# Kernel optimization log

Measured on AMD Instinct MI355X. Metric: run time of the kernel, lower is better.

The kernel has to match this reference:

```python
import jax, jax.numpy as jnp
import numpy as np

N, E, A = 10000, 160000, 8
P, ATTR = 30000, 64
EMB, HID, HEADS = 128, 128, 4
OUT, NF, NR = 64, 1500, 64
HOPS = 3
NEG = -1e30


def _gatv2(x, src, dst, e_emb, node_mask, Wl, Wr, We, att, b):
    """GATv2Conv with edge features, self-loops (edge attr = mean of kept edges),
    restricted to the node subset given by node_mask (mirrors Data.subgraph)."""
    n = x.shape[0]
    H, D = att.shape
    xl = (x @ Wl).reshape(n, H, D)
    xr = (x @ Wr).reshape(n, H, D)
    emask = node_mask[src] & node_mask[dst]
    w = emask.astype(x.dtype)
    mean_e = (e_emb * w[:, None]).sum(0) / jnp.maximum(w.sum(), 1.0)  # fill_value='mean'
    loops = jnp.arange(n)
    src_a = jnp.concatenate([src, loops])
    dst_a = jnp.concatenate([dst, loops])
    e_a = jnp.concatenate([e_emb, jnp.broadcast_to(mean_e, (n, e_emb.shape[1]))], axis=0)
    m_a = jnp.concatenate([emask, node_mask])
    ee = (e_a @ We).reshape(-1, H, D)
    z = jax.nn.leaky_relu(xl[src_a] + xr[dst_a] + ee, 0.2)  # [E+N, H, D]
    s = jnp.einsum('ehd,hd->eh', z, att)
    s = jnp.where(m_a[:, None], s, NEG)
    smax = jax.ops.segment_max(s, dst_a, num_segments=n)
    ex = jnp.exp(s - smax[dst_a]) * m_a[:, None].astype(x.dtype)
    den = jax.ops.segment_sum(ex, dst_a, num_segments=n)
    alpha = ex / (den[dst_a] + 1e-16)
    out = jax.ops.segment_sum(alpha[:, :, None] * xl[src_a], dst_a, num_segments=n)
    return out.reshape(n, H * D) + b


def _softmax_aggr(x, mask):
    # PyG SoftmaxAggregation (t=1): per-channel softmax over nodes, weighted sum.
    logit = jnp.where(mask[:, None], x, NEG)
    return jnp.einsum('nd,nd->d', jax.nn.softmax(logit, axis=0), x)


def _khop(seed, src, dst):
    # k_hop_subgraph, flow='source_to_target': grow node set backwards along edges.
    m = jnp.zeros(N, dtype=bool).at[seed].set(True)
    for _ in range(HOPS):
        reach = jnp.zeros(N, dtype=jnp.int32).at[src].max(m[dst].astype(jnp.int32))
        m = m | (reach > 0)
    return m


def _forward(node_pred, edge_index, edge_attr, arg_nodes, pred_emb, Wl1, Wr1, We1, att1, b1,
             Wl2, Wr2, We2, att2, b2, kqv_f, kqvb_f, kqv_r, kqvb_r, a_rel, m_rel, p_rel,
             aW_f, ab_f, aW_r, ab_r, Wfr, bfr, Wro, bro):
    src, dst = edge_index[0], edge_index[1]
    p_emb = pred_emb[node_pred]   # [N, EMB]
    a_emb = pred_emb[edge_attr]   # [E, EMB] (original uses predicate_embedding for attrs)
    full = jnp.ones(N, dtype=bool)
    h = _gatv2(p_emb, src, dst, a_emb, full, Wl1, Wr1, We1, att1, b1)  # [N, HID*HEADS]
    frame_x = _softmax_aggr(h, full)                                   # [512]
    masks = jax.vmap(lambda s: _khop(s, src, dst))(arg_nodes)          # [A, N]
    role_list = []
    for i in range(A):  # mirrors the original Python loop over root args (A fixed, small)
        hi = _gatv2(h, src, dst, a_emb, masks[i], Wl2, Wr2, We2, att2, b2)
        role_list.append(_softmax_aggr(hi, masks[i]))
    role_x = jnp.stack(role_list)                                      # [A, 512]
    # HGTConv, heads=1. Edge types: 0=f-loop, 1=frame->role, 2=r-loop.
    sq = 1.0 / np.sqrt(OUT)
    kf = frame_x @ kqv_f[0] + kqvb_f[0]
    vf = frame_x @ kqv_f[2] + kqvb_f[2]
    kr = role_x @ kqv_r[0] + kqvb_r[0]
    qr = role_x @ kqv_r[1] + kqvb_r[1]
    vr = role_x @ kqv_r[2] + kqvb_r[2]
    # frame dst has a single incoming edge (f-loop) -> softmax weight is exactly 1
    agg_f = vf @ m_rel[0]
    # role dst: softmax over {frame->role edge, role self-loop}
    s_fr = (qr * (kf @ a_rel[1])[None, :]).sum(-1) * sq * p_rel[1]  # [A]
    s_rr = (qr * (kr @ a_rel[2])).sum(-1) * sq * p_rel[2]           # [A]
    al = jax.nn.softmax(jnp.stack([s_fr, s_rr], axis=1), axis=1)    # [A, 2]
    agg_r = al[:, 0:1] * (vf @ m_rel[1])[None, :] + al[:, 1:2] * (vr @ m_rel[2])
    # in_dim (512) != out_dim (64) -> no residual skip in PyG HGTConv
    out_f = jax.nn.gelu(agg_f, approximate=False) @ aW_f + ab_f
    out_r = jax.nn.gelu(agg_r, approximate=False) @ aW_r + ab_r
    frame = jax.nn.log_softmax(out_f @ Wfr + bfr)
    roles = jax.nn.log_softmax(out_r @ Wro + bro, axis=-1)
    return frame, roles


def setup_inputs() -> dict:
    key = jax.random.key(0)
    ki = iter(jax.random.split(key, 32))
    def nrm(shape, fan):
        return (jax.random.normal(next(ki), shape, jnp.float32) / np.sqrt(fan)).astype(jnp.float32)
    D1 = HID * HEADS
    inp = {
        'node_pred': jax.random.randint(next(ki), (N,), 0, P),
        'edge_index': jax.random.randint(next(ki), (2, E), 0, N),
        'edge_attr': jax.random.randint(next(ki), (E,), 0, ATTR),
        'arg_nodes': jax.random.randint(next(ki), (A,), 0, N),
        'pred_emb': nrm((P, EMB), 1.0),
        'Wl1': nrm((EMB, D1), EMB), 'Wr1': nrm((EMB, D1), EMB), 'We1': nrm((EMB, D1), EMB),
        'att1': nrm((HEADS, HID), HID), 'b1': jnp.zeros((D1,), jnp.float32),
        'Wl2': nrm((D1, D1), D1), 'Wr2': nrm((D1, D1), D1), 'We2': nrm((EMB, D1), EMB),
        'att2': nrm((HEADS, HID), HID), 'b2': jnp.zeros((D1,), jnp.float32),
        'kqv_f': nrm((3, D1, OUT), D1), 'kqvb_f': jnp.zeros((3, OUT), jnp.float32),
        'kqv_r': nrm((3, D1, OUT), D1), 'kqvb_r': jnp.zeros((3, OUT), jnp.float32),
        'a_rel': nrm((3, OUT, OUT), OUT), 'm_rel': nrm((3, OUT, OUT), OUT),
        'p_rel': jnp.ones((3,), jnp.float32),
        'aW_f': nrm((OUT, OUT), OUT), 'ab_f': jnp.zeros((OUT,), jnp.float32),
        'aW_r': nrm((OUT, OUT), OUT), 'ab_r': jnp.zeros((OUT,), jnp.float32),
        'Wfr': nrm((OUT, NF), OUT), 'bfr': jnp.zeros((NF,), jnp.float32),
        'Wro': nrm((OUT, NR), OUT), 'bro': jnp.zeros((NR,), jnp.float32),
    }
    return inp


def reference(node_pred, edge_index, edge_attr, arg_nodes, pred_emb, Wl1, Wr1, We1, att1, b1,
              Wl2, Wr2, We2, att2, b2, kqv_f, kqvb_f, kqv_r, kqvb_r, a_rel, m_rel, p_rel,
              aW_f, ab_f, aW_r, ab_r, Wfr, bfr, Wro, bro):
    return _forward(node_pred, edge_index, edge_attr, arg_nodes, pred_emb, Wl1, Wr1, We1, att1, b1,
                    Wl2, Wr2, We2, att2, b2, kqv_f, kqvb_f, kqv_r, kqvb_r, a_rel, m_rel, p_rel,
                    aW_f, ab_f, aW_r, ab_r, Wfr, bfr, Wro, bro)
```

## Files before the change

### kernel.cpp

```cpp
#include <hip/hip_runtime.h>
#include <cfloat>
#include <cmath>

static constexpr int NN   = 10000;
static constexpr int NE   = 160000;
static constexpr int NA   = 8;
static constexpr int D1   = 512;
static constexpr int EMBD = 128;
static constexpr int NATTR= 64;
static constexpr int OUTD = 64;
static constexpr int NFR  = 1500;
static constexpr int AGG_NB = 250;

typedef short bf16x8 __attribute__((ext_vector_type(8)));
typedef float f32x4  __attribute__((ext_vector_type(4)));

__device__ __forceinline__ float b2f(unsigned short u) {
    union { unsigned u; float f; } v; v.u = ((unsigned)u) << 16; return v.f;
}
__device__ __forceinline__ unsigned short f2b(float f) {
    union { float f; unsigned u; } v; v.f = f;
    unsigned r = v.u + 0x7FFFu + ((v.u >> 16) & 1u);
    return (unsigned short)(r >> 16);
}

__global__ void k_cast_all(const float* __restrict__ W1, const float* __restrict__ W2,
                           const float* __restrict__ W3, const float* __restrict__ W4,
                           unsigned short* __restrict__ o1, unsigned short* __restrict__ o2,
                           unsigned short* __restrict__ o3, unsigned short* __restrict__ o4) {
    int i = blockIdx.x * blockDim.x + threadIdx.x;
    const int n1 = EMBD * D1 / 4;
    const int n2 = D1 * D1 / 4;
    const float* src; unsigned short* dst; int off;
    if (i < n1)                { src = W1; dst = o1; off = i; }
    else if (i < 2 * n1)       { src = W2; dst = o2; off = i - n1; }
    else if (i < 2 * n1 + n2)  { src = W3; dst = o3; off = i - 2 * n1; }
    else if (i < 2 * n1 + 2 * n2) { src = W4; dst = o4; off = i - 2 * n1 - n2; }
    else return;
    float4 v = ((const float4*)src)[off];
    ushort4 o; o.x = f2b(v.x); o.y = f2b(v.y); o.z = f2b(v.z); o.w = f2b(v.w);
    ((ushort4*)dst)[off] = o;
}

__global__ void k_gather_pemb(const int* __restrict__ node_pred,
                              const float* __restrict__ pred_emb,
                              unsigned short* __restrict__ pemb) {
    int idx = blockIdx.x * blockDim.x + threadIdx.x;
    int total = NN * (EMBD / 4);
    if (idx >= total) return;
    int n = idx >> 5, j = idx & 31;
    float4 v = ((const float4*)(pred_emb + (size_t)node_pred[n] * EMBD))[j];
    ushort4 o; o.x = f2b(v.x); o.y = f2b(v.y); o.z = f2b(v.z); o.w = f2b(v.w);
    ((ushort4*)(pemb + (size_t)n * EMBD))[j] = o;
}

__global__ void k_attr_ee(const float* __restrict__ pred_emb,
                          const float* __restrict__ We1, const float* __restrict__ We2,
                          unsigned short* __restrict__ t1, unsigned short* __restrict__ t2) {
    int a = blockIdx.x & 63;
    int which = blockIdx.x >> 6;
    const float* We = which ? We2 : We1;
    unsigned short* out = which ? t2 : t1;
    __shared__ float row[EMBD];
    if (threadIdx.x < EMBD) row[threadIdx.x] = pred_emb[a * EMBD + threadIdx.x];
    __syncthreads();
    int c = threadIdx.x;
    float acc = 0.f;
    for (int k = 0; k < EMBD; ++k) acc += row[k] * We[k * D1 + c];
    out[a * D1 + c] = f2b(acc);
}

__global__ void k_indeg(const int* __restrict__ dst, int* __restrict__ counts) {
    int stride = gridDim.x * blockDim.x;
    for (int e = blockIdx.x * blockDim.x + threadIdx.x; e < NE; e += stride)
        atomicAdd(&counts[dst[e]], 1);
}

__global__ __launch_bounds__(1024) void k_scan(const int* __restrict__ counts,
                                               int* __restrict__ row_ptr,
                                               int* __restrict__ cursor) {
    __shared__ int s[1024];
    __shared__ int base_s;
    int t = threadIdx.x;
    if (t == 0) base_s = 0;
    __syncthreads();
    for (int c0 = 0; c0 < NN; c0 += 1024) {
        int v = (c0 + t < NN) ? counts[c0 + t] : 0;
        s[t] = v; __syncthreads();
        for (int off = 1; off < 1024; off <<= 1) {
            int add = (t >= off) ? s[t - off] : 0;
            __syncthreads();
            s[t] += add;
            __syncthreads();
        }
        int base = base_s;
        int excl = base + s[t] - v;
        if (c0 + t < NN) { row_ptr[c0 + t] = excl; cursor[c0 + t] = excl; }
        __syncthreads();
        if (t == 0) base_s = base + s[1023];
        __syncthreads();
    }
    if (t == 0) row_ptr[NN] = base_s;
}

__global__ void k_scatter(const int* __restrict__ src, const int* __restrict__ dst,
                          const int* __restrict__ attr, int* __restrict__ cursor,
                          int* __restrict__ csr_src, int* __restrict__ csr_attr) {
    int stride = gridDim.x * blockDim.x;
    for (int e = blockIdx.x * blockDim.x + threadIdx.x; e < NE; e += stride) {
        int pos = atomicAdd(&cursor[dst[e]], 1);
        csr_src[pos] = src[e];
        csr_attr[pos] = attr[e];
    }
}

__global__ void k_mask_seed(const int* __restrict__ arg_nodes, unsigned* __restrict__ mask) {
    if (threadIdx.x < NA) atomicOr(&mask[arg_nodes[threadIdx.x]], 1u << threadIdx.x);
}

__global__ void k_prop(const unsigned* __restrict__ oldm, unsigned* __restrict__ newm,
                       const int* __restrict__ src, const int* __restrict__ dst) {
    int stride = gridDim.x * blockDim.x;
    int t0 = blockIdx.x * blockDim.x + threadIdx.x;
    for (int n = t0; n < NN; n += stride) atomicOr(&newm[n], oldm[n]);
    for (int e = t0; e < NE; e += stride) {
        unsigned v = oldm[dst[e]];
        if (v) atomicOr(&newm[src[e]], v);
    }
}

__global__ void k_hist(const int* __restrict__ src, const int* __restrict__ dst,
                       const int* __restrict__ attr, const unsigned* __restrict__ mask,
                       unsigned* __restrict__ hist) {
    __shared__ unsigned lh[9 * 64];
    for (int i = threadIdx.x; i < 9 * 64; i += blockDim.x) lh[i] = 0;
    __syncthreads();
    int stride = gridDim.x * blockDim.x;
    for (int e = blockIdx.x * blockDim.x + threadIdx.x; e < NE; e += stride) {
        int a = attr[e] & 63;
        atomicAdd(&lh[a], 1u);
        unsigned bits = mask[src[e]] & mask[dst[e]];
        while (bits) {
            int i = __ffs(bits) - 1;
            bits &= bits - 1;
            atomicAdd(&lh[(1 + i) * 64 + a], 1u);
        }
    }
    __syncthreads();
    for (int i = threadIdx.x; i < 9 * 64; i += blockDim.x)
        if (lh[i]) atomicAdd(&hist[i], lh[i]);
}

__global__ __launch_bounds__(512) void k_mean_ee(const unsigned* __restrict__ hist,
                                                 const float* __restrict__ pred_emb,
                                                 const float* __restrict__ We1,
                                                 const float* __restrict__ We2,
                                                 unsigned short* __restrict__ mee1,
                                                 unsigned short* __restrict__ mee2) {
    int g = blockIdx.x;
    const float* We = (g == 0) ? We1 : We2;
    unsigned short* out = (g == 0) ? mee1 : (mee2 + (g - 1) * D1);
    __shared__ float cnt[64];
    __shared__ float me[EMBD];
    __shared__ float tot_s;
    if (threadIdx.x < 64) cnt[threadIdx.x] = (float)hist[g * 64 + threadIdx.x];
    __syncthreads();
    if (threadIdx.x == 0) {
        float tt = 0.f;
        for (int a = 0; a < 64; ++a) tt += cnt[a];
        tot_s = fmaxf(tt, 1.0f);
    }
    __syncthreads();
    if (threadIdx.x < EMBD) {
        float acc = 0.f;
        for (int a = 0; a < 64; ++a) acc += cnt[a] * pred_emb[a * EMBD + threadIdx.x];
        me[threadIdx.x] = acc / tot_s;
    }
    __syncthreads();
    int c = threadIdx.x;
    float acc = 0.f;
    for (int k = 0; k < EMBD; ++k) acc += me[k] * We[k * D1 + c];
    out[c] = f2b(acc);
}

__global__ __launch_bounds__(256) void k_gemm_dual(const unsigned short* __restrict__ A,
                                                   const unsigned short* __restrict__ B0,
                                                   const unsigned short* __restrict__ B1,
                                                   unsigned short* __restrict__ C0,
                                                   unsigned short* __restrict__ C1,
                                                   int M, int K, int N) {
    const unsigned short* B = blockIdx.z ? B1 : B0;
    unsigned short* C = blockIdx.z ? C1 : C0;
    __shared__ unsigned short As[64][40];
    __shared__ unsigned short Bs[64][40];
    int tid = threadIdx.x;
    int wave = tid >> 6, lane = tid & 63;
    int bm = blockIdx.y * 64, bn = blockIdx.x * 64;
    int wr = (wave >> 1) * 32, wc = (wave & 1) * 32;
    f32x4 zero = {0.f, 0.f, 0.f, 0.f};
    f32x4 acc[2][2] = {{zero, zero}, {zero, zero}};
    for (int k0 = 0; k0 < K; k0 += 32) {
#pragma unroll
        for (int i = 0; i < 4; ++i) {
            int idx = tid + 256 * i;
            int row = idx >> 4, kp = (idx & 15) * 2;
            unsigned v = 0;
            if (bm + row < M) v = *(const unsigned*)&A[(size_t)(bm + row) * K + k0 + kp];
            *(unsigned*)&As[row][kp] = v;
        }
#pragma unroll
        for (int i = 0; i < 8; ++i) {
            int idx = tid + 256 * i;
            int k = idx >> 6, n = idx & 63;
            Bs[n][k] = B[(size_t)(k0 + k) * N + bn + n];
        }
        __syncthreads();
        int r = lane & 15, kb = (lane >> 4) * 8;
        bf16x8 a0 = *(const bf16x8*)&As[wr + r][kb];
        bf16x8 a1 = *(const bf16x8*)&As[wr + 16 + r][kb];
        bf16x8 b0 = *(const bf16x8*)&Bs[wc + r][kb];
        bf16x8 b1 = *(const bf16x8*)&Bs[wc + 16 + r][kb];
        acc[0][0] = __builtin_amdgcn_mfma_f32_16x16x32_bf16(a0, b0, acc[0][0], 0, 0, 0);
        acc[0][1] = __builtin_amdgcn_mfma_f32_16x16x32_bf16(a0, b1, acc[0][1], 0, 0, 0);
        acc[1][0] = __builtin_amdgcn_mfma_f32_16x16x32_bf16(a1, b0, acc[1][0], 0, 0, 0);
        acc[1][1] = __builtin_amdgcn_mfma_f32_16x16x32_bf16(a1, b1, acc[1][1], 0, 0, 0);
        __syncthreads();
    }
    int cr = (lane >> 4) * 4, cc = lane & 15;
#pragma unroll
    for (int i = 0; i < 2; ++i)
#pragma unroll
        for (int j = 0; j < 2; ++j)
#pragma unroll
            for (int q = 0; q < 4; ++q) {
                int row = bm + wr + i * 16 + cr + q;
                int col = bn + wc + j * 16 + cc;
                if (row < M) C[(size_t)row * N + col] = f2b(acc[i][j][q]);
            }
}

__global__ __launch_bounds__(256) void k_gat(const unsigned short* __restrict__ xl,
                                             const unsigned short* __restrict__ xr,
                                             const unsigned short* __restrict__ attr_ee,
                                             const unsigned short* __restrict__ mean_ee,
                                             const float* __restrict__ att,
                                             const float* __restrict__ bias,
                                             const int* __restrict__ row_ptr,
                                             const int* __restrict__ csr_src,
                                             const int* __restrict__ csr_attr,
                                             unsigned short* __restrict__ out) {
    int n = blockIdx.x;
    int t = threadIdx.x;
    int c = 2 * t;
    unsigned vr_ = *(const unsigned*)&xr[(size_t)n * D1 + c];
    float xr0 = b2f((unsigned short)(vr_ & 0xffff));
    float xr1 = b2f((unsigned short)(vr_ >> 16));
    float a0 = att[c], a1 = att[c + 1];
    float m = -FLT_MAX, den = 0.f, acc0 = 0.f, acc1 = 0.f;
    int pstart = row_ptr[n], pend = row_ptr[n + 1];
    int deg = pend - pstart;
    int items = deg + 1;
    for (int it = 0; it < items; it += 4) {
        float xs0[4], xs1[4], ps[4];
#pragma unroll
        for (int u = 0; u < 4; ++u) {
            int item = it + u;
            bool valid = item < items;
            int s; const unsigned short* ee;
            if (!valid || item == deg) { s = n; ee = mean_ee; }
            else {
                int p = pstart + item;
                s = csr_src[p];
                ee = attr_ee + (size_t)(csr_attr[p] & 63) * D1;
            }
            unsigned vs = *(const unsigned*)&xl[(size_t)s * D1 + c];
            unsigned ve = *(const unsigned*)&ee[c];
            float x0 = b2f((unsigned short)(vs & 0xffff));
            float x1 = b2f((unsigned short)(vs >> 16));
            float z0 = x0 + xr0 + b2f((unsigned short)(ve & 0xffff));
            float z1 = x1 + xr1 + b2f((unsigned short)(ve >> 16));
            z0 = (z0 > 0.f) ? z0 : 0.2f * z0;
            z1 = (z1 > 0.f) ? z1 : 0.2f * z1;
            xs0[u] = x0; xs1[u] = x1;
            ps[u] = z0 * a0 + z1 * a1;
        }
#pragma unroll
        for (int off = 32; off; off >>= 1) {
#pragma unroll
            for (int u = 0; u < 4; ++u) ps[u] += __shfl_xor(ps[u], off, 64);
        }
#pragma unroll
        for (int u = 0; u < 4; ++u) if (it + u >= items) ps[u] = -FLT_MAX;
        float nm = fmaxf(fmaxf(fmaxf(ps[0], ps[1]), fmaxf(ps[2], ps[3])), m);
        float sc = __expf(m - nm);
        float w0 = __expf(ps[0] - nm);
        float w1 = __expf(ps[1] - nm);
        float w2 = __expf(ps[2] - nm);
        float w3 = __expf(ps[3] - nm);
        den  = den * sc + ((w0 + w1) + (w2 + w3));
        acc0 = acc0 * sc + ((w0 * xs0[0] + w1 * xs0[1]) + (w2 * xs0[2] + w3 * xs0[3]));
        acc1 = acc1 * sc + ((w0 * xs1[0] + w1 * xs1[1]) + (w2 * xs1[2] + w3 * xs1[3]));
        m = nm;
    }
    float inv = 1.f / (den + 1e-16f);
    unsigned short o0 = f2b(acc0 * inv + bias[c]);
    unsigned short o1 = f2b(acc1 * inv + bias[c + 1]);
    *(unsigned*)&out[(size_t)n * D1 + c] = ((unsigned)o1 << 16) | o0;
}

__global__ __launch_bounds__(256) void k_gat_m4(const unsigned short* __restrict__ xl,
                                                const unsigned short* __restrict__ xr,
                                                const unsigned short* __restrict__ attr_ee,
                                                const unsigned short* __restrict__ mee,
                                                const float* __restrict__ att,
                                                const float* __restrict__ bias,
                                                const int* __restrict__ row_ptr,
                                                const int* __restrict__ csr_src,
                                                const int* __restrict__ csr_attr,
                                                const unsigned* __restrict__ mask, int bitbase,
                                                unsigned short* __restrict__ o0,
                                                unsigned short* __restrict__ o1,
                                                unsigned short* __restrict__ o2,
                                                unsigned short* __restrict__ o3) {
    int n = blockIdx.x;
    unsigned mb_n = (mask[n] >> bitbase) & 0xFu;
    if (!mb_n) return;
    __shared__ int lst[256];
    __shared__ int lcnt;
    int t = threadIdx.x, lane = t & 63;
    int c = 2 * t;
    unsigned vr_ = *(const unsigned*)&xr[(size_t)n * D1 + c];
    float xr0 = b2f((unsigned short)(vr_ & 0xffff));
    float xr1 = b2f((unsigned short)(vr_ >> 16));
    float a0 = att[c], a1 = att[c + 1];
    float m[4], den[4], ac0[4], ac1[4];
#pragma unroll
    for (int b = 0; b < 4; ++b) { m[b] = -FLT_MAX; den[b] = 0.f; ac0[b] = 0.f; ac1[b] = 0.f; }
    int pstart = row_ptr[n], pend = row_ptr[n + 1];
    for (int p0 = pstart; p0 < pend; p0 += 256) {
        int chunk = min(256, pend - p0);
        __syncthreads();
        if (t == 0) lcnt = 0;
        __syncthreads();
        unsigned bits = 0; int sv = 0, av = 0;
        if (t < chunk) {
            int p = p0 + t;
            sv = csr_src[p];
            av = csr_attr[p] & 63;
            bits = (mask[sv] >> bitbase) & mb_n & 0xFu;
        }
        bool kept = bits != 0;
        unsigned long long bal = __ballot(kept);
        int base = 0;
        if (lane == 0) base = atomicAdd(&lcnt, __popcll(bal));
        base = __shfl(base, 0, 64);
        int pfx = __popcll(bal & ((1ull << lane) - 1));
        if (kept) lst[base + pfx] = sv | (av << 14) | ((int)bits << 20);
        __syncthreads();
        int cnt = lcnt;
        int i = 0;
        for (; i + 1 < cnt; i += 2) {
            int vA = lst[i], vB = lst[i + 1];
            int sA = vA & 0x3FFF, sB = vB & 0x3FFF;
            unsigned bA = ((unsigned)vA >> 20) & 0xF, bB = ((unsigned)vB >> 20) & 0xF;
            const unsigned short* eA = attr_ee + (size_t)((vA >> 14) & 63) * D1;
            const unsigned short* eB = attr_ee + (size_t)((vB >> 14) & 63) * D1;
            unsigned vsA = *(const unsigned*)&xl[(size_t)sA * D1 + c];
            unsigned veA = *(const unsigned*)&eA[c];
            unsigned vsB = *(const unsigned*)&xl[(size_t)sB * D1 + c];
            unsigned veB = *(const unsigned*)&eB[c];
            float xA0 = b2f((unsigned short)(vsA & 0xffff)), xA1 = b2f((unsigned short)(vsA >> 16));
            float xB0 = b2f((unsigned short)(vsB & 0xffff)), xB1 = b2f((unsigned short)(vsB >> 16));
            float zA0 = xA0 + xr0 + b2f((unsigned short)(veA & 0xffff));
            float zA1 = xA1 + xr1 + b2f((unsigned short)(veA >> 16));
            float zB0 = xB0 + xr0 + b2f((unsigned short)(veB & 0xffff));
            float zB1 = xB1 + xr1 + b2f((unsigned short)(veB >> 16));
            zA0 = (zA0 > 0.f) ? zA0 : 0.2f * zA0;
            zA1 = (zA1 > 0.f) ? zA1 : 0.2f * zA1;
            zB0 = (zB0 > 0.f) ? zB0 : 0.2f * zB0;
            zB1 = (zB1 > 0.f) ? zB1 : 0.2f * zB1;
            float pa = zA0 * a0 + zA1 * a1;
            float pb = zB0 * a0 + zB1 * a1;
#pragma unroll
            for (int off = 32; off; off >>= 1) {
                pa += __shfl_xor(pa, off, 64);
                pb += __shfl_xor(pb, off, 64);
            }
#pragma unroll
            for (int b = 0; b < 4; ++b) {
                if (!(((bA | bB) >> b) & 1)) continue;
                float pae = ((bA >> b) & 1) ? pa : -FLT_MAX;
                float pbe = ((bB >> b) & 1) ? pb : -FLT_MAX;
                float nm = fmaxf(m[b], fmaxf(pae, pbe));
                float sc = __expf(m[b] - nm);
                float wa = __expf(pae - nm);
                float wb = __expf(pbe - nm);
                den[b] = den[b] * sc + wa + wb;
                ac0[b] = ac0[b] * sc + wa * xA0 + wb * xB0;
                ac1[b] = ac1[b] * sc + wa * xA1 + wb * xB1;
                m[b] = nm;
            }
        }
        if (i < cnt) {
            int vA = lst[i];
            int sA = vA & 0x3FFF;
            unsigned bA = ((unsigned)vA >> 20) & 0xF;
            const unsigned short* eA = attr_ee + (size_t)((vA >> 14) & 63) * D1;
            unsigned vsA = *(const unsigned*)&xl[(size_t)sA * D1 + c];
            unsigned veA = *(const unsigned*)&eA[c];
            float xA0 = b2f((unsigned short)(vsA & 0xffff)), xA1 = b2f((unsigned short)(vsA >> 16));
            float zA0 = xA0 + xr0 + b2f((unsigned short)(veA & 0xffff));
            float zA1 = xA1 + xr1 + b2f((unsigned short)(veA >> 16));
            zA0 = (zA0 > 0.f) ? zA0 : 0.2f * zA0;
            zA1 = (zA1 > 0.f) ? zA1 : 0.2f * zA1;
            float pa = zA0 * a0 + zA1 * a1;
#pragma unroll
            for (int off = 32; off; off >>= 1) pa += __shfl_xor(pa, off, 64);
#pragma unroll
            for (int b = 0; b < 4; ++b) {
                if (!((bA >> b) & 1)) continue;
                float nm = fmaxf(m[b], pa);
                float sc = __expf(m[b] - nm);
                float wa = __expf(pa - nm);
                den[b] = den[b] * sc + wa;
                ac0[b] = ac0[b] * sc + wa * xA0;
                ac1[b] = ac1[b] * sc + wa * xA1;
                m[b] = nm;
            }
        }
    }
    unsigned vsn = *(const unsigned*)&xl[(size_t)n * D1 + c];
    float xn0 = b2f((unsigned short)(vsn & 0xffff)), xn1 = b2f((unsigned short)(vsn >> 16));
    float bi0 = bias[c], bi1 = bias[c + 1];
#pragma unroll
    for (int b = 0; b < 4; ++b) {
        if (!((mb_n >> b) & 1)) continue;
        unsigned ve = *(const unsigned*)&mee[(size_t)b * D1 + c];
        float z0 = xn0 + xr0 + b2f((unsigned short)(ve & 0xffff));
        float z1 = xn1 + xr1 + b2f((unsigned short)(ve >> 16));
        z0 = (z0 > 0.f) ? z0 : 0.2f * z0;
        z1 = (z1 > 0.f) ? z1 : 0.2f * z1;
        float ps = z0 * a0 + z1 * a1;
#pragma unroll
        for (int off = 32; off; off >>= 1) ps += __shfl_xor(ps, off, 64);
        float nm = fmaxf(m[b], ps);
        float sc = __expf(m[b] - nm);
        float w  = __expf(ps - nm);
        float dd = den[b] * sc + w;
        float A0 = ac0[b] * sc + w * xn0;
        float A1 = ac1[b] * sc + w * xn1;
        float inv = 1.f / (dd + 1e-16f);
        unsigned short q0 = f2b(A0 * inv + bi0);
        unsigned short q1 = f2b(A1 * inv + bi1);
        unsigned pk = ((unsigned)q1 << 16) | q0;
        unsigned short* ob = (b == 0) ? o0 : (b == 1) ? o1 : (b == 2) ? o2 : o3;
        *(unsigned*)&ob[(size_t)n * D1 + c] = pk;
    }
}

__global__ __launch_bounds__(512) void k_aggr_partial(const unsigned short* __restrict__ x,
                                                      float* __restrict__ part) {
// ... 239 lines not shown
    const float* att1 = (const float*)d_in[8];
    const float* b1  = (const float*)d_in[9];
    const float* Wl2 = (const float*)d_in[10];
    const float* Wr2 = (const float*)d_in[11];
    const float* We2 = (const float*)d_in[12];
    const float* att2 = (const float*)d_in[13];
    const float* b2  = (const float*)d_in[14];
    const float* kqv_f  = (const float*)d_in[15];
    const float* kqvb_f = (const float*)d_in[16];
    const float* kqv_r  = (const float*)d_in[17];
    const float* kqvb_r = (const float*)d_in[18];
    const float* a_rel  = (const float*)d_in[19];
    const float* m_rel  = (const float*)d_in[20];
    const float* p_rel  = (const float*)d_in[21];
    const float* aW_f = (const float*)d_in[22];
    const float* ab_f = (const float*)d_in[23];
    const float* aW_r = (const float*)d_in[24];
    const float* ab_r = (const float*)d_in[25];
    const float* Wfr = (const float*)d_in[26];
    const float* bfr = (const float*)d_in[27];
    const float* Wro = (const float*)d_in[28];
    const float* bro = (const float*)d_in[29];
    float* outp = (float*)d_out;

    char* base = (char*)d_ws;
    size_t off = 0;
    auto alloc = [&](size_t bytes) -> void* {
        void* p = base + off;
        off += (bytes + 255) & ~(size_t)255;
        return p;
    };
    float* frame_x = (float*)alloc(D1 * 4);
    float* role_x  = (float*)alloc(NA * D1 * 4);
    float* part    = (float*)alloc((size_t)4 * AGG_NB * 3 * D1 * 4);
    float* kf   = (float*)alloc(64 * 4);
    float* vf   = (float*)alloc(64 * 4);
    float* kr   = (float*)alloc(512 * 4);
    float* qr   = (float*)alloc(512 * 4);
    float* vr   = (float*)alloc(512 * 4);
    float* outf = (float*)alloc(64 * 4);
    float* outr = (float*)alloc(512 * 4);
    float* flog = (float*)alloc(NFR * 4);
    int* row_ptr  = (int*)alloc((NN + 1) * 4);
    int* cursor   = (int*)alloc(NN * 4);
    unsigned* maskA = (unsigned*)alloc(NN * 4);
    unsigned* maskB = (unsigned*)alloc(NN * 4);
    unsigned* maskC = (unsigned*)alloc(NN * 4);
    unsigned* hist  = (unsigned*)alloc(9 * 64 * 4);
    size_t zero_end = off;
    size_t zero_beg = (char*)cursor - base;
    int* csr_src  = (int*)alloc((size_t)NE * 4);
    int* csr_attr = (int*)alloc((size_t)NE * 4);
    unsigned short* xl    = (unsigned short*)alloc((size_t)NN * D1 * 2);
    unsigned short* xr_   = (unsigned short*)alloc((size_t)NN * D1 * 2);
    unsigned short* hbuf  = (unsigned short*)alloc((size_t)NN * D1 * 2);
    unsigned short* hi1   = (unsigned short*)alloc((size_t)NN * D1 * 2);
    unsigned short* hi2   = (unsigned short*)alloc((size_t)NN * D1 * 2);
    unsigned short* hi3   = (unsigned short*)alloc((size_t)NN * D1 * 2);
    unsigned short* pemb  = (unsigned short*)alloc((size_t)NN * EMBD * 2);
    unsigned short* wl1b  = (unsigned short*)alloc((size_t)EMBD * D1 * 2);
    unsigned short* wr1b  = (unsigned short*)alloc((size_t)EMBD * D1 * 2);
    unsigned short* wl2b  = (unsigned short*)alloc((size_t)D1 * D1 * 2);
    unsigned short* wr2b  = (unsigned short*)alloc((size_t)D1 * D1 * 2);
    unsigned short* attr1 = (unsigned short*)alloc((size_t)NATTR * D1 * 2);
    unsigned short* attr2 = (unsigned short*)alloc((size_t)NATTR * D1 * 2);
    unsigned short* mee1  = (unsigned short*)alloc(D1 * 2);
    unsigned short* mee2  = (unsigned short*)alloc((size_t)NA * D1 * 2);

    hipMemsetAsync(base + zero_beg, 0, zero_end - zero_beg, stream);
    k_cast_all<<<640, 256, 0, stream>>>(Wl1, Wr1, Wl2, Wr2, wl1b, wr1b, wl2b, wr2b);
    k_gather_pemb<<<(NN * (EMBD / 4) + 255) / 256, 256, 0, stream>>>(node_pred, pred_emb, pemb);
    k_attr_ee<<<128, 512, 0, stream>>>(pred_emb, We1, We2, attr1, attr2);
    k_indeg<<<256, 256, 0, stream>>>(e_dst, cursor);
    k_scan<<<1, 1024, 0, stream>>>(cursor, row_ptr, cursor);
    k_scatter<<<256, 256, 0, stream>>>(e_src, e_dst, edge_attr, cursor, csr_src, csr_attr);

    dim3 gg(D1 / 64, (NN + 63) / 64, 2);
    k_gemm_dual<<<gg, 256, 0, stream>>>(pemb, wl1b, wr1b, xl, xr_, NN, EMBD, D1);

    k_mask_seed<<<1, 64, 0, stream>>>(arg_nodes, maskA);
    k_prop<<<256, 256, 0, stream>>>(maskA, maskB, e_src, e_dst);
    k_prop<<<256, 256, 0, stream>>>(maskB, maskC, e_src, e_dst);
    k_prop<<<256, 256, 0, stream>>>(maskC, maskA, e_src, e_dst);

    k_hist<<<256, 256, 0, stream>>>(e_src, e_dst, edge_attr, maskA, hist);
    k_mean_ee<<<9, 512, 0, stream>>>(hist, pred_emb, We1, We2, mee1, mee2);

    k_gat<<<NN, 256, 0, stream>>>(xl, xr_, attr1, mee1, att1, b1,
                                  row_ptr, csr_src, csr_attr, hbuf);
    k_aggr_partial<<<AGG_NB, 512, 0, stream>>>(hbuf, part);
    k_combine_w<<<64, 512, 0, stream>>>(part, AGG_NB, 1, frame_x);

    k_gemm_dual<<<gg, 256, 0, stream>>>(hbuf, wl2b, wr2b, xl, xr_, NN, D1, D1);

    for (int pb = 0; pb < 2; ++pb) {
        int bb = pb * 4;
        k_gat_m4<<<NN, 256, 0, stream>>>(xl, xr_, attr2, mee2 + (size_t)bb * D1, att2, b2,
                                         row_ptr, csr_src, csr_attr, maskA, bb,
                                         hbuf, hi1, hi2, hi3);
        k_aggr_partial4<<<AGG_NB, 512, 0, stream>>>(hbuf, hi1, hi2, hi3, maskA, bb, part);
        k_combine_w<<<256, 512, 0, stream>>>(part, AGG_NB, 4, role_x + (size_t)bb * D1);
    }

    k_hgt_a<<<26, 64, 0, stream>>>(frame_x, role_x, kqv_f, kqvb_f, kqv_r, kqvb_r,
                                   kf, vf, kr, qr, vr);
    k_hgt_b<<<1, 512, 0, stream>>>(kf, vf, kr, qr, vr, a_rel, m_rel, p_rel,
                                   aW_f, ab_f, aW_r, ab_r, outf, outr);
    k_frame_logits<<<(NFR + 255) / 256, 256, 0, stream>>>(outf, Wfr, bfr, flog);
    k_final<<<1, 512, 0, stream>>>(flog, outr, Wro, bro, outp);
}
```

Measured before the change: 420.7 us.

## Fuse prep kernels, prefilter masked edges per group, enlarge GEMM tiles

Merges weight casting, embedding gather, attribute projection, in-degree counting and mask seeding into one launch, and replaces the serial block scan with a warp-shuffle scan. Packs src and attr into one int per CSR entry. Builds a second, filtered CSR per 4-argument group that holds only edges kept by the k-hop mask, so the layer-2 GAT kernel walks only relevant edges and processes them four at a time. The GEMM moves to 128x128 tiles, and the two group combine launches become one. The cost is extra histogram, scan and scatter passes plus larger partial buffers.

```diff
diff --git a/kernel.cpp b/kernel.cpp
--- a/kernel.cpp
+++ b/kernel.cpp
@@ -24,98 +24,114 @@
     return (unsigned short)(r >> 16);
 }
 
-__global__ void k_cast_all(const float* __restrict__ W1, const float* __restrict__ W2,
-                           const float* __restrict__ W3, const float* __restrict__ W4,
-                           unsigned short* __restrict__ o1, unsigned short* __restrict__ o2,
-                           unsigned short* __restrict__ o3, unsigned short* __restrict__ o4) {
-    int i = blockIdx.x * blockDim.x + threadIdx.x;
-    const int n1 = EMBD * D1 / 4;
-    const int n2 = D1 * D1 / 4;
-    const float* src; unsigned short* dst; int off;
-    if (i < n1)                { src = W1; dst = o1; off = i; }
-    else if (i < 2 * n1)       { src = W2; dst = o2; off = i - n1; }
-    else if (i < 2 * n1 + n2)  { src = W3; dst = o3; off = i - 2 * n1; }
-    else if (i < 2 * n1 + 2 * n2) { src = W4; dst = o4; off = i - 2 * n1 - n2; }
-    else return;
-    float4 v = ((const float4*)src)[off];
-    ushort4 o; o.x = f2b(v.x); o.y = f2b(v.y); o.z = f2b(v.z); o.w = f2b(v.w);
-    ((ushort4*)dst)[off] = o;
-}
-
-__global__ void k_gather_pemb(const int* __restrict__ node_pred,
-                              const float* __restrict__ pred_emb,
-                              unsigned short* __restrict__ pemb) {
-    int idx = blockIdx.x * blockDim.x + threadIdx.x;
-    int total = NN * (EMBD / 4);
-    if (idx >= total) return;
-    int n = idx >> 5, j = idx & 31;
-    float4 v = ((const float4*)(pred_emb + (size_t)node_pred[n] * EMBD))[j];
-    ushort4 o; o.x = f2b(v.x); o.y = f2b(v.y); o.z = f2b(v.z); o.w = f2b(v.w);
-    ((ushort4*)(pemb + (size_t)n * EMBD))[j] = o;
-}
-
-__global__ void k_attr_ee(const float* __restrict__ pred_emb,
-                          const float* __restrict__ We1, const float* __restrict__ We2,
-                          unsigned short* __restrict__ t1, unsigned short* __restrict__ t2) {
-    int a = blockIdx.x & 63;
-    int which = blockIdx.x >> 6;
-    const float* We = which ? We2 : We1;
-    unsigned short* out = which ? t2 : t1;
-    __shared__ float row[EMBD];
-    if (threadIdx.x < EMBD) row[threadIdx.x] = pred_emb[a * EMBD + threadIdx.x];
-    __syncthreads();
-    int c = threadIdx.x;
-    float acc = 0.f;
-    for (int k = 0; k < EMBD; ++k) acc += row[k] * We[k * D1 + c];
-    out[a * D1 + c] = f2b(acc);
-}
-
-__global__ void k_indeg(const int* __restrict__ dst, int* __restrict__ counts) {
-    int stride = gridDim.x * blockDim.x;
-    for (int e = blockIdx.x * blockDim.x + threadIdx.x; e < NE; e += stride)
-        atomicAdd(&counts[dst[e]], 1);
-}
-
-__global__ __launch_bounds__(1024) void k_scan(const int* __restrict__ counts,
-                                               int* __restrict__ row_ptr,
-                                               int* __restrict__ cursor) {
-    __shared__ int s[1024];
-    __shared__ int base_s;
-    int t = threadIdx.x;
-    if (t == 0) base_s = 0;
-    __syncthreads();
-    for (int c0 = 0; c0 < NN; c0 += 1024) {
-        int v = (c0 + t < NN) ? counts[c0 + t] : 0;
-        s[t] = v; __syncthreads();
-        for (int off = 1; off < 1024; off <<= 1) {
-            int add = (t >= off) ? s[t - off] : 0;
-            __syncthreads();
-            s[t] += add;
-            __syncthreads();
-        }
-        int base = base_s;
-        int excl = base + s[t] - v;
-        if (c0 + t < NN) { row_ptr[c0 + t] = excl; cursor[c0 + t] = excl; }
+__global__ __launch_bounds__(512) void k_prep(const float* __restrict__ pred_emb,
+                                              const float* __restrict__ We1,
+                                              const float* __restrict__ We2,
+                                              const float* __restrict__ Wl1,
+                                              const float* __restrict__ Wr1,
+                                              const float* __restrict__ Wl2,
+                                              const float* __restrict__ Wr2,
+                                              const int* __restrict__ node_pred,
+                                              const int* __restrict__ e_dst,
+                                              const int* __restrict__ arg_nodes,
+                                              unsigned short* __restrict__ attr1,
+                                              unsigned short* __restrict__ attr2,
+                                              unsigned short* __restrict__ wl1b,
+                                              unsigned short* __restrict__ wr1b,
+                                              unsigned short* __restrict__ wl2b,
+                                              unsigned short* __restrict__ wr2b,
+                                              unsigned short* __restrict__ pemb,
+                                              int* __restrict__ counts,
+                                              unsigned* __restrict__ maskA) {
+    int b = blockIdx.x, t = threadIdx.x;
+    if (b < 128) {
+        int a = b & 63;
+        const float* We = (b >> 6) ? We2 : We1;
+        unsigned short* out = (b >> 6) ? attr2 : attr1;
+        __shared__ float row[EMBD];
+        if (t < EMBD) row[t] = pred_emb[a * EMBD + t];
         __syncthreads();
-        if (t == 0) base_s = base + s[1023];
-        __syncthreads();
-    }
-    if (t == 0) row_ptr[NN] = base_s;
+        float acc = 0.f;
+        for (int k = 0; k < EMBD; ++k) acc += row[k] * We[k * D1 + t];
+        out[a * D1 + t] = f2b(acc);
+    } else if (b < 448) {
+        int i = (b - 128) * 512 + t;
+        const int n1 = EMBD * D1 / 4, n2 = D1 * D1 / 4;
+        const float* src; unsigned short* dst; int off;
+        if (i < n1)                   { src = Wl1; dst = wl1b; off = i; }
+        else if (i < 2 * n1)          { src = Wr1; dst = wr1b; off = i - n1; }
+        else if (i < 2 * n1 + n2)     { src = Wl2; dst = wl2b; off = i - 2 * n1; }
+        else                          { src = Wr2; dst = wr2b; off = i - 2 * n1 - n2; }
+        float4 v = ((const float4*)src)[off];
+        ushort4 o; o.x = f2b(v.x); o.y = f2b(v.y); o.z = f2b(v.z); o.w = f2b(v.w);
+        ((ushort4*)dst)[off] = o;
+    } else if (b < 1073) {
+        int idx = (b - 448) * 512 + t;
+        int n = idx >> 5, j = idx & 31;
+        float4 v = ((const float4*)(pred_emb + (size_t)node_pred[n] * EMBD))[j];
+        ushort4 o; o.x = f2b(v.x); o.y = f2b(v.y); o.z = f2b(v.z); o.w = f2b(v.w);
+        ((ushort4*)(pemb + (size_t)n * EMBD))[j] = o;
+    } else if (b < 1173) {
+        int id = (b - 1073) * 512 + t;
+        for (int e = id; e < NE; e += 100 * 512) atomicAdd(&counts[e_dst[e]], 1);
+    } else {
+        if (t < NA) atomicOr(&maskA[arg_nodes[t]], 1u << t);
+    }
+}
+
+template <int CE>
+__global__ __launch_bounds__(1024) void k_scan_g(const int* __restrict__ counts, int n,
+                                                 int* __restrict__ row_ptr,
+                                                 int* __restrict__ cursor) {
+    __shared__ int wsum[16];
+    __shared__ int total_s;
+    int t = threadIdx.x, lane = t & 63, w = t >> 6;
+    int base = t * CE;
+    int v[CE];
+    int s = 0;
+#pragma unroll
+    for (int j = 0; j < CE; ++j) {
+        int idx = base + j;
+        int x = (idx < n) ? counts[idx] : 0;
+        v[j] = s; s += x;
+    }
+    int inc = s;
+#pragma unroll
+    for (int off = 1; off < 64; off <<= 1) {
+        int u = __shfl_up(inc, off, 64);
+        if (lane >= off) inc += u;
+    }
+    if (lane == 63) wsum[w] = inc;
+    __syncthreads();
+    if (w == 0 && lane < 16) {
+        int ws = wsum[lane];
+        int wi = ws;
+#pragma unroll
+        for (int off = 1; off < 16; off <<= 1) {
+            int u = __shfl_up(wi, off, 64);
+            if (lane >= off) wi += u;
+        }
+        wsum[lane] = wi - ws;
+        if (lane == 15) total_s = wi;
+    }
+    __syncthreads();
+    int excl = wsum[w] + (inc - s);
+#pragma unroll
+    for (int j = 0; j < CE; ++j) {
+        int idx = base + j;
+        if (idx < n) { int val = excl + v[j]; row_ptr[idx] = val; cursor[idx] = val; }
+    }
+    if (t == 0) row_ptr[n] = total_s;
 }
 
 __global__ void k_scatter(const int* __restrict__ src, const int* __restrict__ dst,
                           const int* __restrict__ attr, int* __restrict__ cursor,
-                          int* __restrict__ csr_src, int* __restrict__ csr_attr) {
+                          int* __restrict__ csr_pack) {
     int stride = gridDim.x * blockDim.x;
     for (int e = blockIdx.x * blockDim.x + threadIdx.x; e < NE; e += stride) {
         int pos = atomicAdd(&cursor[dst[e]], 1);
-        csr_src[pos] = src[e];
-        csr_attr[pos] = attr[e];
-    }
-}
-
-__global__ void k_mask_seed(const int* __restrict__ arg_nodes, unsigned* __restrict__ mask) {
-    if (threadIdx.x < NA) atomicOr(&mask[arg_nodes[threadIdx.x]], 1u << threadIdx.x);
+        csr_pack[pos] = src[e] | ((attr[e] & 63) << 14);
+    }
 }
 
 __global__ void k_prop(const unsigned* __restrict__ oldm, unsigned* __restrict__ newm,
@@ -129,9 +145,9 @@
     }
 }
 
-__global__ void k_hist(const int* __restrict__ src, const int* __restrict__ dst,
-                       const int* __restrict__ attr, const unsigned* __restrict__ mask,
-                       unsigned* __restrict__ hist) {
+__global__ void k_hist2(const int* __restrict__ src, const int* __restrict__ dst,
+                        const int* __restrict__ attr, const unsigned* __restrict__ mask,
+                        unsigned* __restrict__ hist, int* __restrict__ fc) {
     __shared__ unsigned lh[9 * 64];
     for (int i = threadIdx.x; i < 9 * 64; i += blockDim.x) lh[i] = 0;
     __syncthreads();
@@ -140,6 +156,8 @@
         int a = attr[e] & 63;
         atomicAdd(&lh[a], 1u);
         unsigned bits = mask[src[e]] & mask[dst[e]];
+        if (bits & 0xFu)  atomicAdd(&fc[dst[e]], 1);
+        if (bits >> 4)    atomicAdd(&fc[NN + dst[e]], 1);
         while (bits) {
             int i = __ffs(bits) - 1;
             bits &= bits - 1;
@@ -149,6 +167,20 @@
     __syncthreads();
     for (int i = threadIdx.x; i < 9 * 64; i += blockDim.x)
         if (lh[i]) atomicAdd(&hist[i], lh[i]);
+}
+
+__global__ void k_fscatter(const int* __restrict__ src, const int* __restrict__ dst,
+                           const int* __restrict__ attr, const unsigned* __restrict__ mask,
+                           int* __restrict__ fcur, int* __restrict__ fpack) {
+    int stride = gridDim.x * blockDim.x;
+    for (int e = blockIdx.x * blockDim.x + threadIdx.x; e < NE; e += stride) {
+        unsigned b8 = mask[src[e]] & mask[dst[e]];
+        if (!b8) continue;
+        int pk = src[e] | ((attr[e] & 63) << 14);
+        unsigned g0 = b8 & 0xFu, g1 = (b8 >> 4) & 0xFu;
+        if (g0) { int pos = atomicAdd(&fcur[dst[e]], 1);      fpack[pos] = pk | (int)(g0 << 20); }
+        if (g1) { int pos = atomicAdd(&fcur[NN + dst[e]], 1); fpack[pos] = pk | (int)(g1 << 20); }
+    }
 }
 
 __global__ __launch_bounds__(512) void k_mean_ee(const unsigned* __restrict__ hist,
@@ -183,25 +215,25 @@
     out[c] = f2b(acc);
 }
 
-__global__ __launch_bounds__(256) void k_gemm_dual(const unsigned short* __restrict__ A,
-                                                   const unsigned short* __restrict__ B0,
-                                                   const unsigned short* __restrict__ B1,
-                                                   unsigned short* __restrict__ C0,
-                                                   unsigned short* __restrict__ C1,
-                                                   int M, int K, int N) {
+__global__ __launch_bounds__(256) void k_gemm128(const unsigned short* __restrict__ A,
+                                                 const unsigned short* __restrict__ B0,
+                                                 const unsigned short* __restrict__ B1,
+                                                 unsigned short* __restrict__ C0,
+                                                 unsigned short* __restrict__ C1,
+                                                 int M, int K, int N) {
     const unsigned short* B = blockIdx.z ? B1 : B0;
     unsigned short* C = blockIdx.z ? C1 : C0;
-    __shared__ unsigned short As[64][40];
-    __shared__ unsigned short Bs[64][40];
+    __shared__ unsigned short As[128][40];
+    __shared__ unsigned short Bs[128][40];
     int tid = threadIdx.x;
     int wave = tid >> 6, lane = tid & 63;
-    int bm = blockIdx.y * 64, bn = blockIdx.x * 64;
-    int wr = (wave >> 1) * 32, wc = (wave & 1) * 32;
-    f32x4 zero = {0.f, 0.f, 0.f, 0.f};
-    f32x4 acc[2][2] = {{zero, zero}, {zero, zero}};
+    int bm = blockIdx.y * 128, bn = blockIdx.x * 128;
+    int wr = (wave >> 1) * 64, wc = (wave & 1) * 64;
+    int r = lane & 15, kb = (lane >> 4) * 8;
+    f32x4 acc[4][4] = {};
     for (int k0 = 0; k0 < K; k0 += 32) {
 #pragma unroll
-        for (int i = 0; i < 4; ++i) {
+        for (int i = 0; i < 8; ++i) {
             int idx = tid + 256 * i;
             int row = idx >> 4, kp = (idx & 15) * 2;
             unsigned v = 0;
@@ -211,26 +243,29 @@
 #pragma unroll
         for (int i = 0; i < 8; ++i) {
             int idx = tid + 256 * i;
-            int k = idx >> 6, n = idx & 63;
-            Bs[n][k] = B[(size_t)(k0 + k) * N + bn + n];
+            int k = idx >> 6, n2 = (idx & 63) * 2;
+            unsigned v = *(const unsigned*)&B[(size_t)(k0 + k) * N + bn + n2];
+            Bs[n2][k]     = (unsigned short)(v & 0xffff);
+            Bs[n2 + 1][k] = (unsigned short)(v >> 16);
         }
         __syncthreads();
-        int r = lane & 15, kb = (lane >> 4) * 8;
-        bf16x8 a0 = *(const bf16x8*)&As[wr + r][kb];
-        bf16x8 a1 = *(const bf16x8*)&As[wr + 16 + r][kb];
-        bf16x8 b0 = *(const bf16x8*)&Bs[wc + r][kb];
-        bf16x8 b1 = *(const bf16x8*)&Bs[wc + 16 + r][kb];
-        acc[0][0] = __builtin_amdgcn_mfma_f32_16x16x32_bf16(a0, b0, acc[0][0], 0, 0, 0);
-        acc[0][1] = __builtin_amdgcn_mfma_f32_16x16x32_bf16(a0, b1, acc[0][1], 0, 0, 0);
-        acc[1][0] = __builtin_amdgcn_mfma_f32_16x16x32_bf16(a1, b0, acc[1][0], 0, 0, 0);
-        acc[1][1] = __builtin_amdgcn_mfma_f32_16x16x32_bf16(a1, b1, acc[1][1], 0, 0, 0);
+        bf16x8 a[4], bb[4];
+#pragma unroll
+        for (int i = 0; i < 4; ++i) a[i]  = *(const bf16x8*)&As[wr + i * 16 + r][kb];
+#pragma unroll
+        for (int j = 0; j < 4; ++j) bb[j] = *(const bf16x8*)&Bs[wc + j * 16 + r][kb];
+#pragma unroll
+        for (int i = 0; i < 4; ++i)
+#pragma unroll
+            for (int j = 0; j < 4; ++j)
+                acc[i][j] = __builtin_amdgcn_mfma_f32_16x16x32_bf16(a[i], bb[j], acc[i][j], 0, 0, 0);
         __syncthreads();
     }
     int cr = (lane >> 4) * 4, cc = lane & 15;
 #pragma unroll
-    for (int i = 0; i < 2; ++i)
-#pragma unroll
-        for (int j = 0; j < 2; ++j)
+    for (int i = 0; i < 4; ++i)
+#pragma unroll
+        for (int j = 0; j < 4; ++j)
 #pragma unroll
             for (int q = 0; q < 4; ++q) {
                 int row = bm + wr + i * 16 + cr + q;
@@ -246,8 +281,7 @@
                                              const float* __restrict__ att,
                                              const float* __restrict__ bias,
                                              const int* __restrict__ row_ptr,
-                                             const int* __restrict__ csr_src,
-                                             const int* __restrict__ csr_attr,
+                                             const int* __restrict__ csr_pack,
                                              unsigned short* __restrict__ out) {
     int n = blockIdx.x;
     int t = threadIdx.x;
@@ -269,9 +303,9 @@
             int s; const unsigned short* ee;
             if (!valid || item == deg) { s = n; ee = mean_ee; }
             else {
-                int p = pstart + item;
-                s = csr_src[p];
-                ee = attr_ee + (size_t)(csr_attr[p] & 63) * D1;
+                int v = csr_pack[pstart + item];
+                s = v & 0x3FFF;
+                ee = attr_ee + (size_t)((v >> 14) & 63) * D1;
             }
             unsigned vs = *(const unsigned*)&xl[(size_t)s * D1 + c];
             unsigned ve = *(const unsigned*)&ee[c];
@@ -308,26 +342,25 @@
     *(unsigned*)&out[(size_t)n * D1 + c] = ((unsigned)o1 << 16) | o0;
 }
 
-__global__ __launch_bounds__(256) void k_gat_m4(const unsigned short* __restrict__ xl,
-                                                const unsigned short* __restrict__ xr,
-                                                const unsigned short* __restrict__ attr_ee,
-                                                const unsigned short* __restrict__ mee,
-                                                const float* __restrict__ att,
-                                                const float* __restrict__ bias,
-                                                const int* __restrict__ row_ptr,
-                                                const int* __restrict__ csr_src,
-                                                const int* __restrict__ csr_attr,
-                                                const unsigned* __restrict__ mask, int bitbase,
-                                                unsigned short* __restrict__ o0,
-                                                unsigned short* __restrict__ o1,
-                                                unsigned short* __restrict__ o2,
-                                                unsigned short* __restrict__ o3) {
+__global__ __launch_bounds__(256) void k_gat_f(const unsigned short* __restrict__ xl,
+                                               const unsigned short* __restrict__ xr,
+                                               const unsigned short* __restrict__ attr_ee,
+                                               const unsigned short* __restrict__ mee,
+                                               const float* __restrict__ att,
+                                               const float* __restrict__ bias,
+                                               const int* __restrict__ frp,
+                                               const int* __restrict__ fpack,
+                                               const unsigned* __restrict__ mask,
+                                               int gi,
+                                               unsigned short* __restrict__ o0,
+                                               unsigned short* __restrict__ o1,
+                                               unsigned short* __restrict__ o2,
+                                               unsigned short* __restrict__ o3) {
     int n = blockIdx.x;
+    int bitbase = gi * 4;
     unsigned mb_n = (mask[n] >> bitbase) & 0xFu;
     if (!mb_n) return;
-    __shared__ int lst[256];
-    __shared__ int lcnt;
-    int t = threadIdx.x, lane = t & 63;
+    int t = threadIdx.x;
     int c = 2 * t;
     unsigned vr_ = *(const unsigned*)&xr[(size_t)n * D1 + c];
     float xr0 = b2f((unsigned short)(vr_ & 0xffff));
@@ -336,97 +369,52 @@
     float m[4], den[4], ac0[4], ac1[4];
 #pragma unroll
     for (int b = 0; b < 4; ++b) { m[b] = -FLT_MAX; den[b] = 0.f; ac0[b] = 0.f; ac1[b] = 0.f; }
-    int pstart = row_ptr[n], pend = row_ptr[n + 1];
-    for (int p0 = pstart; p0 < pend; p0 += 256) {
-        int chunk = min(256, pend - p0);
-        __syncthreads();
-        if (t == 0) lcnt = 0;
-        __syncthreads();
-        unsigned bits = 0; int sv = 0, av = 0;
-        if (t < chunk) {
-            int p = p0 + t;
-            sv = csr_src[p];
-            av = csr_attr[p] & 63;
-            bits = (mask[sv] >> bitbase) & mb_n & 0xFu;
-        }
-        bool kept = bits != 0;
-        unsigned long long bal = __ballot(kept);
-        int base = 0;
-        if (lane == 0) base = atomicAdd(&lcnt, __popcll(bal));
-        base = __shfl(base, 0, 64);
-        int pfx = __popcll(bal & ((1ull << lane) - 1));
-        if (kept) lst[base + pfx] = sv | (av << 14) | ((int)bits << 20);
-        __syncthreads();
-        int cnt = lcnt;
-        int i = 0;
-        for (; i + 1 < cnt; i += 2) {
-            int vA = lst[i], vB = lst[i + 1];
-            int sA = vA & 0x3FFF, sB = vB & 0x3FFF;
-            unsigned bA = ((unsigned)vA >> 20) & 0xF, bB = ((unsigned)vB >> 20) & 0xF;
-            const unsigned short* eA = attr_ee + (size_t)((vA >> 14) & 63) * D1;
-            const unsigned short* eB = attr_ee + (size_t)((vB >> 14) & 63) * D1;
-            unsigned vsA = *(const unsigned*)&xl[(size_t)sA * D1 + c];
-            unsigned veA = *(const unsigned*)&eA[c];
-            unsigned vsB = *(const unsigned*)&xl[(size_t)sB * D1 + c];
-            unsigned veB = *(const unsigned*)&eB[c];
-            float xA0 = b2f((unsigned short)(vsA & 0xffff)), xA1 = b2f((unsigned short)(vsA >> 16));
-            float xB0 = b2f((unsigned short)(vsB & 0xffff)), xB1 = b2f((unsigned short)(vsB >> 16));
-            float zA0 = xA0 + xr0 + b2f((unsigned short)(veA & 0xffff));
-            float zA1 = xA1 + xr1 + b2f((unsigned short)(veA >> 16));
-            float zB0 = xB0 + xr0 + b2f((unsigned short)(veB & 0xffff));
-            float zB1 = xB1 + xr1 + b2f((unsigned short)(veB >> 16));
-            zA0 = (zA0 > 0.f) ? zA0 : 0.2f * zA0;
-            zA1 = (zA1 > 0.f) ? zA1 : 0.2f * zA1;
-            zB0 = (zB0 > 0.f) ? zB0 : 0.2f * zB0;
-            zB1 = (zB1 > 0.f) ? zB1 : 0.2f * zB1;
-            float pa = zA0 * a0 + zA1 * a1;
-            float pb = zB0 * a0 + zB1 * a1;
-#pragma unroll
-            for (int off = 32; off; off >>= 1) {
-                pa += __shfl_xor(pa, off, 64);
-                pb += __shfl_xor(pb, off, 64);
-            }
-#pragma unroll
-            for (int b = 0; b < 4; ++b) {
-                if (!(((bA | bB) >> b) & 1)) continue;
-                float pae = ((bA >> b) & 1) ? pa : -FLT_MAX;
-                float pbe = ((bB >> b) & 1) ? pb : -FLT_MAX;
-                float nm = fmaxf(m[b], fmaxf(pae, pbe));
-                float sc = __expf(m[b] - nm);
-                float wa = __expf(pae - nm);
-                float wb = __expf(pbe - nm);
-                den[b] = den[b] * sc + wa + wb;
-                ac0[b] = ac0[b] * sc + wa * xA0 + wb * xB0;
-                ac1[b] = ac1[b] * sc + wa * xA1 + wb * xB1;
-                m[b] = nm;
-            }
-        }
-        if (i < cnt) {
-            int vA = lst[i];
-            int sA = vA & 0x3FFF;
-            unsigned bA = ((unsigned)vA >> 20) & 0xF;
-            const unsigned short* eA = attr_ee + (size_t)((vA >> 14) & 63) * D1;
-            unsigned vsA = *(const unsigned*)&xl[(size_t)sA * D1 + c];
-            unsigned veA = *(const unsigned*)&eA[c];
-            float xA0 = b2f((unsigned short)(vsA & 0xffff)), xA1 = b2f((unsigned short)(vsA >> 16));
-            float zA0 = xA0 + xr0 + b2f((unsigned short)(veA & 0xffff));
-            float zA1 = xA1 + xr1 + b2f((unsigned short)(veA >> 16));
-            zA0 = (zA0 > 0.f) ? zA0 : 0.2f * zA0;
-            zA1 = (zA1 > 0.f) ? zA1 : 0.2f * zA1;
-            float pa = zA0 * a0 + zA1 * a1;
-#pragma unroll
-            for (int off = 32; off; off >>= 1) pa += __shfl_xor(pa, off, 64);
-#pragma unroll
-            for (int b = 0; b < 4; ++b) {
-                if (!((bA >> b) & 1)) continue;
-                float nm = fmaxf(m[b], pa);
-                float sc = __expf(m[b] - nm);
-                float wa = __expf(pa - nm);
-                den[b] = den[b] * sc + wa;
-                ac0[b] = ac0[b] * sc + wa * xA0;
-                ac1[b] = ac1[b] * sc + wa * xA1;
-                m[b] = nm;
-            }
+    int p0 = frp[gi * NN + n], p1 = frp[gi * NN + n + 1];
+    for (int it = p0; it < p1; it += 4) {
+        float xs0[4], xs1[4], ps[4];
+        unsigned eb[4];
+#pragma unroll
+        for (int u = 0; u < 4; ++u) {
+            int p = it + u;
+            bool valid = p < p1;
+            int v = valid ? fpack[p] : 0;
+            eb[u] = valid ? ((unsigned)v >> 20) & 0xFu : 0u;
+            int s = v & 0x3FFF;
+            const unsigned short* ee = attr_ee + (size_t)((v >> 14) & 63) * D1;
+            unsigned vs = *(const unsigned*)&xl[(size_t)s * D1 + c];
+            unsigned ve = *(const unsigned*)&ee[c];
+            float x0 = b2f((unsigned short)(vs & 0xffff));
+            float x1 = b2f((unsigned short)(vs >> 16));
+            float z0 = x0 + xr0 + b2f((unsigned short)(ve & 0xffff));
+            float z1 = x1 + xr1 + b2f((unsigned short)(ve >> 16));
+            z0 = (z0 > 0.f) ? z0 : 0.2f * z0;
+            z1 = (z1 > 0.f) ? z1 : 0.2f * z1;
+            xs0[u] = x0; xs1[u] = x1;
+            ps[u] = z0 * a0 + z1 * a1;
+        }
+#pragma unroll
+        for (int off = 32; off; off >>= 1) {
+#pragma unroll
+            for (int u = 0; u < 4; ++u) ps[u] += __shfl_xor(ps[u], off, 64);
+        }
+        unsigned ub = eb[0] | eb[1] | eb[2] | eb[3];
+#pragma unroll
+        for (int b = 0; b < 4; ++b) {
+            if (!((ub >> b) & 1)) continue;
+            float p0e = ((eb[0] >> b) & 1) ? ps[0] : -FLT_MAX;
+            float p1e = ((eb[1] >> b) & 1) ? ps[1] : -FLT_MAX;
+            float p2e = ((eb[2] >> b) & 1) ? ps[2] : -FLT_MAX;
+            float p3e = ((eb[3] >> b) & 1) ? ps[3] : -FLT_MAX;
+            float nm = fmaxf(fmaxf(fmaxf(p0e, p1e), fmaxf(p2e, p3e)), m[b]);
+            float sc = __expf(m[b] - nm);
+            float w0 = __expf(p0e - nm);
+            float w1 = __expf(p1e - nm);
+            float w2 = __expf(p2e - nm);
+            float w3 = __expf(p3e - nm);
+            den[b] = den[b] * sc + ((w0 + w1) + (w2 + w3));
+            ac0[b] = ac0[b] * sc + ((w0 * xs0[0] + w1 * xs0[1]) + (w2 * xs0[2] + w3 * xs0[3]));
+            ac1[b] = ac1[b] * sc + ((w0 * xs1[0] + w1 * xs1[1]) + (w2 * xs1[2] + w3 * xs1[3]));
+            m[b] = nm;
         }
     }
     unsigned vsn = *(const unsigned*)&xl[(size_t)n * D1 + c];
@@ -732,7 +720,7 @@
     };
     float* frame_x = (float*)alloc(D1 * 4);
     float* role_x  = (float*)alloc(NA * D1 * 4);
-    float* part    = (float*)alloc((size_t)4 * AGG_NB * 3 * D1 * 4);
+    float* part    = (float*)alloc((size_t)8 * AGG_NB * 3 * D1 * 4);
     float* kf   = (float*)alloc(64 * 4);
     float* vf   = (float*)alloc(64 * 4);
     float* kr   = (float*)alloc(512 * 4);
@@ -742,15 +730,18 @@
     float* outr = (float*)alloc(512 * 4);
     float* flog = (float*)alloc(NFR * 4);
     int* row_ptr  = (int*)alloc((NN + 1) * 4);
+    int* frp      = (int*)alloc((2 * NN + 1) * 4);
+    int* fcur     = (int*)alloc((size_t)2 * NN * 4);
     int* cursor   = (int*)alloc(NN * 4);
     unsigned* maskA = (unsigned*)alloc(NN * 4);
     unsigned* maskB = (unsigned*)alloc(NN * 4);
     unsigned* maskC = (unsigned*)alloc(NN * 4);
     unsigned* hist  = (unsigned*)alloc(9 * 64 * 4);
+    int* fc         = (int*)alloc((size_t)2 * NN * 4);
     size_t zero_end = off;
     size_t zero_beg = (char*)cursor - base;
-    int* csr_src  = (int*)alloc((size_t)NE * 4);
-    int* csr_attr = (int*)alloc((size_t)NE * 4);
+    int* csr_pack = (int*)alloc((size_t)NE * 4);
+    int* fpack    = (int*)alloc((size_t)2 * NE * 4);
     unsigned short* xl    = (unsigned short*)alloc((size_t)NN * D1 * 2);
     unsigned short* xr_   = (unsigned short*)alloc((size_t)NN * D1 * 2);
     unsigned short* hbuf  = (unsigned short*)alloc((size_t)NN * D1 * 2);
@@ -768,39 +759,40 @@
     unsigned short* mee2  = (unsigned short*)alloc((size_t)NA * D1 * 2);
 
     hipMemsetAsync(base + zero_beg, 0, zero_end - zero_beg, stream);
-    k_cast_all<<<640, 256, 0, stream>>>(Wl1, Wr1, Wl2, Wr2, wl1b, wr1b, wl2b, wr2b);
-    k_gather_pemb<<<(NN * (EMBD / 4) + 255) / 256, 256, 0, stream>>>(node_pred, pred_emb, pemb);
-    k_attr_ee<<<128, 512, 0, stream>>>(pred_emb, We1, We2, attr1, attr2);
-    k_indeg<<<256, 256, 0, stream>>>(e_dst, cursor);
-    k_scan<<<1, 1024, 0, stream>>>(cursor, row_ptr, cursor);
-    k_scatter<<<256, 256, 0, stream>>>(e_src, e_dst, edge_attr, cursor, csr_src, csr_attr);
-
-    dim3 gg(D1 / 64, (NN + 63) / 64, 2);
-    k_gemm_dual<<<gg, 256, 0, stream>>>(pemb, wl1b, wr1b, xl, xr_, NN, EMBD, D1);
-
-    k_mask_seed<<<1, 64, 0, stream>>>(arg_nodes, maskA);
+    k_prep<<<1174, 512, 0, stream>>>(pred_emb, We1, We2, Wl1, Wr1, Wl2, Wr2,
+                                     node_pred, e_dst, arg_nodes,
+                                     attr1, attr2, wl1b, wr1b, wl2b, wr2b,
+                                     pemb, cursor, maskA);
+    k_scan_g<10><<<1, 1024, 0, stream>>>(cursor, NN, row_ptr, cursor);
+    k_scatter<<<256, 256, 0, stream>>>(e_src, e_dst, edge_attr, cursor, csr_pack);
+
+    dim3 gg(D1 / 128, (NN + 127) / 128, 2);
+    k_gemm128<<<gg, 256, 0, stream>>>(pemb, wl1b, wr1b, xl, xr_, NN, EMBD, D1);
+
     k_prop<<<256, 256, 0, stream>>>(maskA, maskB, e_src, e_dst);
     k_prop<<<256, 256, 0, stream>>>(maskB, maskC, e_src, e_dst);
     k_prop<<<256, 256, 0, stream>>>(maskC, maskA, e_src, e_dst);
 
-    k_hist<<<256, 256, 0, stream>>>(e_src, e_dst, edge_attr, maskA, hist);
+    k_hist2<<<256, 256, 0, stream>>>(e_src, e_dst, edge_attr, maskA, hist, fc);
     k_mean_ee<<<9, 512, 0, stream>>>(hist, pred_emb, We1, We2, mee1, mee2);
+    k_scan_g<20><<<1, 1024, 0, stream>>>(fc, 2 * NN, frp, fcur);
+    k_fscatter<<<256, 256, 0, stream>>>(e_src, e_dst, edge_attr, maskA, fcur, fpack);
 
     k_gat<<<NN, 256, 0, stream>>>(xl, xr_, attr1, mee1, att1, b1,
-                                  row_ptr, csr_src, csr_attr, hbuf);
+                                  row_ptr, csr_pack, hbuf);
     k_aggr_partial<<<AGG_NB, 512, 0, stream>>>(hbuf, part);
     k_combine_w<<<64, 512, 0, stream>>>(part, AGG_NB, 1, frame_x);
 
-    k_gemm_dual<<<gg, 256, 0, stream>>>(hbuf, wl2b, wr2b, xl, xr_, NN, D1, D1);
-
-    for (int pb = 0; pb < 2; ++pb) {
-        int bb = pb * 4;
-        k_gat_m4<<<NN, 256, 0, stream>>>(xl, xr_, attr2, mee2 + (size_t)bb * D1, att2, b2,
-                                         row_ptr, csr_src, csr_attr, maskA, bb,
-                                         hbuf, hi1, hi2, hi3);
-        k_aggr_partial4<<<AGG_NB, 512, 0, stream>>>(hbuf, hi1, hi2, hi3, maskA, bb, part);
-        k_combine_w<<<256, 512, 0, stream>>>(part, AGG_NB, 4, role_x + (size_t)bb * D1);
-    }
+    k_gemm128<<<gg, 256, 0, stream>>>(hbuf, wl2b, wr2b, xl, xr_, NN, D1, D1);
+
+    for (int gi = 0; gi < 2; ++gi) {
+        k_gat_f<<<NN, 256, 0, stream>>>(xl, xr_, attr2, mee2 + (size_t)gi * 4 * D1, att2, b2,
+                                        frp, fpack, maskA, gi,
+                                        hbuf, hi1, hi2, hi3);
+        k_aggr_partial4<<<AGG_NB, 512, 0, stream>>>(hbuf, hi1, hi2, hi3, maskA, gi * 4,
+                                                    part + (size_t)gi * 4 * AGG_NB * 3 * D1);
+    }
+    k_combine_w<<<512, 512, 0, stream>>>(part, AGG_NB, 8, role_x);
 
     k_hgt_a<<<26, 64, 0, stream>>>(frame_x, role_x, kqv_f, kqvb_f, kqv_r, kqvb_r,
                                    kf, vf, kr, qr, vr);
```

After: 434.6 us. +3.3%, slower.
